# Kernel optimization log

Measured on AMD Instinct MI355X. Metric: run time of the kernel, lower is better.

Reference implementation:

```python
import jax, jax.numpy as jnp
import numpy as np

B, Q, S, D = 16, 2048, 2048, 128  # batch(*heads), q_len, kv seq_len, dim_q_k == dim_v


def setup_inputs() -> dict:
    key = jax.random.key(0)
    k1, k2, k3, k4 = jax.random.split(key, 4)
    value = jax.random.normal(k1, (B, S, D), dtype=jnp.float32)
    k_ = jax.random.normal(k2, (B, S, D), dtype=jnp.float32)
    query = jax.random.normal(k3, (B, Q, D), dtype=jnp.float32)
    mask = jax.random.bernoulli(k4, 0.5, (B, Q, S))  # True = illegal connection
    return {"value": value, "key": k_, "query": query, "mask": mask}


def reference(value, key, query, mask):
    scale = np.power(D, -0.5).astype(np.float32)
    # adjacency: [B, Q, S]
    adjacency = jnp.einsum('bqd,bsd->bqs', query, key) * scale
    adjacency = jnp.where(mask, -jnp.inf, adjacency)
    attention = jax.nn.softmax(adjacency, axis=2)
    out = jnp.einsum('bqs,bsd->bqd', attention, value)
    return (out, attention)
```

## Files before the change

### kernel.cpp

```cpp
#include <hip/hip_runtime.h>
#include <hip/hip_bf16.h>

#define B_ 16
#define Q_ 2048
#define S_ 2048
#define D_ 128
#define SCALE 0.08838834764831845f

typedef unsigned short ushort_t;
typedef unsigned long long u64_t;
typedef __attribute__((ext_vector_type(8))) __bf16 bf16x8;
typedef __attribute__((ext_vector_type(8))) short short8;
typedef __attribute__((ext_vector_type(4))) float floatx4;

static __device__ __forceinline__ ushort_t bf16_of_f32(float f) {
    __hip_bfloat16 h = __float2bfloat16(f);
    return *reinterpret_cast<ushort_t*>(&h);
}
static __device__ __forceinline__ float f32_of_bf16(ushort_t u) {
    return __uint_as_float(((unsigned int)u) << 16);
}

__global__ void detect_kernel(const unsigned int* __restrict__ m,
                              const unsigned int* __restrict__ q,
                              int* __restrict__ flags) {
    __shared__ int sI32, sF32, sF16, sCnt;
    int t = threadIdx.x;
    if (t == 0) { sI32 = 0; sF32 = 0; sF16 = 0; sCnt = 0; }
    __syncthreads();
    int notI32 = 0, notF32 = 0, notF16 = 0;
    for (int i = t; i < 1024; i += 256) {
        unsigned int v = m[i];
        if (v & ~1u) notI32 = 1;
        if (!(v == 0u || v == 0x3F800000u)) notF32 = 1;
        unsigned int h0 = v & 0xFFFFu, h1 = v >> 16;
        if (!(h0 == 0u || h0 == 0x3F80u || h0 == 0x3C00u)) notF16 = 1;
        if (!(h1 == 0u || h1 == 0x3F80u || h1 == 0x3C00u)) notF16 = 1;
    }
    int cnt = 0;
    for (int i = t; i < 4096; i += 256) {
        unsigned int lo = q[i] & 0xFFFFu;
        unsigned int e = (lo >> 7) & 0xFFu;
        if (lo == 0u || (e >= 100u && e <= 140u)) cnt++;
    }
    if (notI32) atomicOr(&sI32, 1);
    if (notF32) atomicOr(&sF32, 1);
    if (notF16) atomicOr(&sF16, 1);
    atomicAdd(&sCnt, cnt);
    __syncthreads();
    if (t == 0) {
        int w;
        if (!sI32)      w = 4;
        else if (!sF32) w = 4;
        else if (!sF16) w = 2;
        else            w = 1;
        flags[0] = w;
        flags[1] = (sCnt >= 3276) ? 0 : 1;
    }
}

__global__ void pack_mask_kernel(const void* __restrict__ maskp,
                                 const int* __restrict__ flags,
                                 u64_t* __restrict__ bits) {
    const int mw = flags[0];
    const size_t base = (size_t)blockIdx.x * (256 * 32);
    const int lane = threadIdx.x & 63;
    const int wid  = threadIdx.x >> 6;
    const unsigned int*  m32 = (const unsigned int*)maskp;
    const ushort_t*      m16 = (const ushort_t*)maskp;
    const unsigned char* m8  = (const unsigned char*)maskp;
    #pragma unroll 4
    for (int k = 0; k < 32; ++k) {
        int it = wid + 4 * k;
        size_t idx = base + (size_t)it * 64 + lane;
        bool mk;
        if (mw == 4)      mk = m32[idx] != 0u;
        else if (mw == 2) mk = m16[idx] != 0;
        else              mk = m8[idx]  != 0;
        u64_t b = __ballot(mk);
        if (lane == 0) bits[base / 64 + it] = b;
    }
}

__global__ void transpose_v_kernel(const void* __restrict__ Vraw,
                                   const int* __restrict__ flags,
                                   ushort_t* __restrict__ Vt) {
    __shared__ ushort_t t[32][33];
    const int dt = flags[1];
    int b = blockIdx.z;
    int sb = blockIdx.x * 32, db = blockIdx.y * 32;
    int x = threadIdx.x, y = threadIdx.y;
    ushort_t* Vtb = Vt + (size_t)b * D_ * S_;
    if (dt == 0) {
        const ushort_t* Vb = (const ushort_t*)Vraw + (size_t)b * S_ * D_;
        #pragma unroll
        for (int i = 0; i < 32; i += 8)
            t[y + i][x] = Vb[(size_t)(sb + y + i) * D_ + db + x];
    } else {
        const float* Vb = (const float*)Vraw + (size_t)b * S_ * D_;
        #pragma unroll
        for (int i = 0; i < 32; i += 8)
            t[y + i][x] = bf16_of_f32(Vb[(size_t)(sb + y + i) * D_ + db + x]);
    }
    __syncthreads();
    #pragma unroll
    for (int i = 0; i < 32; i += 8)
        Vtb[(size_t)(db + y + i) * S_ + sb + x] = t[x][y + i];
}

static __device__ __forceinline__ void stage_K(ushort_t (*Kl)[136],
                                               const void* Kraw, int dt,
                                               int b, int s0, int tid) {
    if (dt == 0) {
        const ushort_t* Kg = (const ushort_t*)Kraw;
        #pragma unroll
        for (int j = 0; j < 4; ++j) {
            int i = tid + 256 * j;
            int row = i >> 4, colg = i & 15;
            *(short8*)(&Kl[row][colg * 8]) =
                *(const short8*)(Kg + (size_t)(b * S_ + s0 + row) * D_ + colg * 8);
        }
    } else {
        const float* Kg = (const float*)Kraw;
        #pragma unroll
        for (int j = 0; j < 4; ++j) {
            int i = tid + 256 * j;
            int row = i >> 4, colg = i & 15;
            const float* src = Kg + (size_t)(b * S_ + s0 + row) * D_ + colg * 8;
            float4 f0 = *(const float4*)(src);
            float4 f1 = *(const float4*)(src + 4);
            short8 w;
            w[0] = (short)bf16_of_f32(f0.x); w[1] = (short)bf16_of_f32(f0.y);
            w[2] = (short)bf16_of_f32(f0.z); w[3] = (short)bf16_of_f32(f0.w);
            w[4] = (short)bf16_of_f32(f1.x); w[5] = (short)bf16_of_f32(f1.y);
            w[6] = (short)bf16_of_f32(f1.z); w[7] = (short)bf16_of_f32(f1.w);
            *(short8*)(&Kl[row][colg * 8]) = w;
        }
    }
}

__launch_bounds__(256, 2)
__global__ void attn_fused_kernel(const void* __restrict__ Kraw,
                                  const void* __restrict__ Qraw,
                                  const u64_t* __restrict__ bits,
                                  const int* __restrict__ flags,
                                  const ushort_t* __restrict__ Vt,
                                  void* __restrict__ out_base) {
    __shared__ ushort_t Kl[64][136];
    __shared__ ushort_t Vl[128][72];
    __shared__ ushort_t El[64][72];

    const int tid  = threadIdx.x;
    const int wave = tid >> 6;
    const int lane = tid & 63;
    const int quad = lane >> 4;
    const int c    = lane & 15;

    const int qt = blockIdx.x, b = blockIdx.y;
    const int q0 = qt * 64;
    const int dt = flags[1];

    ushort_t* outh  = (ushort_t*)out_base;
    float*    outf  = (float*)out_base;
    ushort_t* attnh = outh + (size_t)B_ * Q_ * D_;
    float*    attnf = outf + (size_t)B_ * Q_ * D_;

    const size_t rowbase = (size_t)b * Q_ + q0;
    const int myrow = wave * 16 + quad * 4;
    const u64_t* bitrow = bits + (((rowbase + myrow) * (size_t)S_) >> 6);

    bf16x8 qf[4];
    {
        const size_t qrow = rowbase + wave * 16 + c;
        if (dt == 0) {
            const ushort_t* p = (const ushort_t*)Qraw + qrow * D_;
            #pragma unroll
            for (int kk = 0; kk < 4; ++kk)
                qf[kk] = *(const bf16x8*)(p + kk * 32 + quad * 8);
        } else {
            const float* p = (const float*)Qraw + qrow * D_;
            #pragma unroll
            for (int kk = 0; kk < 4; ++kk) {
                float4 f0 = *(const float4*)(p + kk * 32 + quad * 8);
                float4 f1 = *(const float4*)(p + kk * 32 + quad * 8 + 4);
                bf16x8 w;
                w[0] = (__bf16)f0.x; w[1] = (__bf16)f0.y;
                w[2] = (__bf16)f0.z; w[3] = (__bf16)f0.w;
                w[4] = (__bf16)f1.x; w[5] = (__bf16)f1.y;
                w[6] = (__bf16)f1.z; w[7] = (__bf16)f1.w;
                qf[kk] = w;
            }
        }
    }

    floatx4 accO[8];
    #pragma unroll
    for (int i = 0; i < 8; ++i) accO[i] = (floatx4){0.f, 0.f, 0.f, 0.f};
    float lacc[4] = {0.f, 0.f, 0.f, 0.f};

    for (int s0 = 0; s0 < S_; s0 += 64) {
        u64_t bw[4];
        #pragma unroll
        for (int r = 0; r < 4; ++r) bw[r] = bitrow[r * 32 + (s0 >> 6)];

        __syncthreads();
        stage_K(Kl, Kraw, dt, b, s0, tid);
        #pragma unroll
        for (int j = 0; j < 4; ++j) {
            int i = tid + 256 * j;
            int row = i >> 3, colg = i & 7;
            *(short8*)(&Vl[row][colg * 8]) =
                *(const short8*)(Vt + (size_t)(b * D_ + row) * S_ + s0 + colg * 8);
        }
        __syncthreads();

        #pragma unroll
        for (int st = 0; st < 4; ++st) {
            floatx4 acc = (floatx4){0.f, 0.f, 0.f, 0.f};
            #pragma unroll
            for (int kk = 0; kk < 4; ++kk) {
                bf16x8 bf = *(const bf16x8*)(&Kl[st * 16 + c][kk * 32 + quad * 8]);
                acc = __builtin_amdgcn_mfma_f32_16x16x32_bf16(qf[kk], bf, acc, 0, 0, 0);
            }
            #pragma unroll
            for (int r = 0; r < 4; ++r) {
                bool masked = (bw[r] >> (st * 16 + c)) & 1ull;
                float e = masked ? 0.f : __expf(acc[r] * SCALE);
                lacc[r] += e;
                El[myrow + r][st * 16 + c] = bf16_of_f32(e);
            }
        }
        #pragma unroll
        for (int ks = 0; ks < 2; ++ks) {
            bf16x8 af = *(const bf16x8*)(&El[wave * 16 + c][ks * 32 + quad * 8]);
            #pragma unroll
            for (int nt = 0; nt < 8; ++nt) {
                bf16x8 bv = *(const bf16x8*)(&Vl[nt * 16 + c][ks * 32 + quad * 8]);
                accO[nt] = __builtin_amdgcn_mfma_f32_16x16x32_bf16(af, bv, accO[nt], 0, 0, 0);
            }
        }
    }

    float rcpl[4];
    #pragma unroll
    for (int r = 0; r < 4; ++r) {
        float v = lacc[r];
        v += __shfl_xor(v, 1); v += __shfl_xor(v, 2);
        v += __shfl_xor(v, 4); v += __shfl_xor(v, 8);
        rcpl[r] = 1.0f / fmaxf(v, 1e-30f);
    }

    #pragma unroll
    for (int r = 0; r < 4; ++r) {
        size_t orow = (rowbase + myrow + r) * D_;
        #pragma unroll
        for (int nt = 0; nt < 8; ++nt) {
            float v = accO[nt][r] * rcpl[r];
            if (dt == 0) outh[orow + nt * 16 + c] = bf16_of_f32(v);
            else         outf[orow + nt * 16 + c] = v;
        }
    }

    for (int s0 = 0; s0 < S_; s0 += 64) {
        u64_t bw[4];
        #pragma unroll
        for (int r = 0; r < 4; ++r) bw[r] = bitrow[r * 32 + (s0 >> 6)];

        __syncthreads();
        stage_K(Kl, Kraw, dt, b, s0, tid);
        __syncthreads();

        #pragma unroll
        for (int st = 0; st < 4; ++st) {
            floatx4 acc = (floatx4){0.f, 0.f, 0.f, 0.f};
            #pragma unroll
            for (int kk = 0; kk < 4; ++kk) {
                bf16x8 bf = *(const bf16x8*)(&Kl[st * 16 + c][kk * 32 + quad * 8]);
                acc = __builtin_amdgcn_mfma_f32_16x16x32_bf16(qf[kk], bf, acc, 0, 0, 0);
            }
            #pragma unroll
            for (int r = 0; r < 4; ++r) {
                bool masked = (bw[r] >> (st * 16 + c)) & 1ull;
                float e = masked ? 0.f : __expf(acc[r] * SCALE) * rcpl[r];
                El[myrow + r][st * 16 + c] = bf16_of_f32(e);
            }
        }
        __syncthreads();

        #pragma unroll
        for (int j = 0; j < 2; ++j) {
            int s = tid + 256 * j;
            int row = s >> 3, sc = s & 7;
            short8 v = *(short8*)(&El[row][sc * 8]);
            size_t gidx = (rowbase + row) * (size_t)S_ + s0 + sc * 8;
            if (dt == 0) {
                *(short8*)(attnh + gidx) = v;
            } else {
                float4 f0, f1;
                f0.x = f32_of_bf16((ushort_t)v[0]); f0.y = f32_of_bf16((ushort_t)v[1]);
                f0.z = f32_of_bf16((ushort_t)v[2]); f0.w = f32_of_bf16((ushort_t)v[3]);
                f1.x = f32_of_bf16((ushort_t)v[4]); f1.y = f32_of_bf16((ushort_t)v[5]);
                f1.z = f32_of_bf16((ushort_t)v[6]); f1.w = f32_of_bf16((ushort_t)v[7]);
                *(float4*)(attnf + gidx) = f0;
                *(float4*)(attnf + gidx + 4) = f1;
            }
        }
    }
}

extern "C" void kernel_launch(void* const* d_in, const int* in_sizes, int n_in,
                              void* d_out, int out_size, void* d_ws, size_t ws_size,
                              hipStream_t stream) {
    const void* Vraw = d_in[0];
    const void* Kraw = d_in[1];
    const void* Qraw = d_in[2];
    const void* maskp = d_in[3];

    char* ws = (char*)d_ws;
    int*  flags = (int*)ws;
    ushort_t* Vt = (ushort_t*)(ws + 256);
    u64_t* bits  = (u64_t*)(ws + 256 + (size_t)B_ * D_ * S_ * 2);

    detect_kernel<<<1, 256, 0, stream>>>((const unsigned int*)maskp,
                                         (const unsigned int*)Qraw, flags);
    pack_mask_kernel<<<(unsigned int)(((size_t)B_ * Q_ * S_) / 8192), 256, 0, stream>>>(
        maskp, flags, bits);
    transpose_v_kernel<<<dim3(S_ / 32, D_ / 32, B_), dim3(32, 8), 0, stream>>>(
        Vraw, flags, Vt);
    attn_fused_kernel<<<dim3(Q_ / 64, B_), 256, 0, stream>>>(
        Kraw, Qraw, bits, flags, Vt, d_out);
}
```

Measured before the change: 688.5 us.

## Fuse mask packing into attention kernel, pre-convert K to bf16, split S across wave pairs

Removes the separate mask-packing kernel. The fused kernel now stages raw mask tiles in shared memory during the first pass, uses them directly and writes packed bits for the second pass to reuse. K is converted to bf16 once by a new kernel, so both passes load bf16 K directly. Blocks grow to 512 threads, with wave pairs splitting each 64-column S tile and their partial row sums and outputs reduced through shared memory. This trades extra shared memory, more synchronisation and a cross-wave output reduction for fewer passes over the mask and K.

New measurement: 605.2 us. 12.1% less time.

```diff
diff --git a/kernel.cpp b/kernel.cpp
--- a/kernel.cpp
+++ b/kernel.cpp
@@ -59,27 +59,19 @@
     }
 }
 
-__global__ void pack_mask_kernel(const void* __restrict__ maskp,
-                                 const int* __restrict__ flags,
-                                 u64_t* __restrict__ bits) {
-    const int mw = flags[0];
-    const size_t base = (size_t)blockIdx.x * (256 * 32);
-    const int lane = threadIdx.x & 63;
-    const int wid  = threadIdx.x >> 6;
-    const unsigned int*  m32 = (const unsigned int*)maskp;
-    const ushort_t*      m16 = (const ushort_t*)maskp;
-    const unsigned char* m8  = (const unsigned char*)maskp;
-    #pragma unroll 4
-    for (int k = 0; k < 32; ++k) {
-        int it = wid + 4 * k;
-        size_t idx = base + (size_t)it * 64 + lane;
-        bool mk;
-        if (mw == 4)      mk = m32[idx] != 0u;
-        else if (mw == 2) mk = m16[idx] != 0;
-        else              mk = m8[idx]  != 0;
-        u64_t b = __ballot(mk);
-        if (lane == 0) bits[base / 64 + it] = b;
-    }
+__global__ void convert_bf16_kernel(const float* __restrict__ src,
+                                    const int* __restrict__ flags,
+                                    ushort_t* __restrict__ dst) {
+    if (flags[1] == 0) return;
+    size_t i = ((size_t)blockIdx.x * 256 + threadIdx.x) * 8;
+    float4 f0 = *(const float4*)(src + i);
+    float4 f1 = *(const float4*)(src + i + 4);
+    short8 w;
+    w[0] = (short)bf16_of_f32(f0.x); w[1] = (short)bf16_of_f32(f0.y);
+    w[2] = (short)bf16_of_f32(f0.z); w[3] = (short)bf16_of_f32(f0.w);
+    w[4] = (short)bf16_of_f32(f1.x); w[5] = (short)bf16_of_f32(f1.y);
+    w[6] = (short)bf16_of_f32(f1.z); w[7] = (short)bf16_of_f32(f1.w);
+    *(short8*)(dst + i) = w;
 }
 
 __global__ void transpose_v_kernel(const void* __restrict__ Vraw,
@@ -108,57 +100,37 @@
         Vtb[(size_t)(db + y + i) * S_ + sb + x] = t[x][y + i];
 }
 
-static __device__ __forceinline__ void stage_K(ushort_t (*Kl)[136],
-                                               const void* Kraw, int dt,
-                                               int b, int s0, int tid) {
-    if (dt == 0) {
-        const ushort_t* Kg = (const ushort_t*)Kraw;
-        #pragma unroll
-        for (int j = 0; j < 4; ++j) {
-            int i = tid + 256 * j;
-            int row = i >> 4, colg = i & 15;
-            *(short8*)(&Kl[row][colg * 8]) =
-                *(const short8*)(Kg + (size_t)(b * S_ + s0 + row) * D_ + colg * 8);
-        }
-    } else {
-        const float* Kg = (const float*)Kraw;
-        #pragma unroll
-        for (int j = 0; j < 4; ++j) {
-            int i = tid + 256 * j;
-            int row = i >> 4, colg = i & 15;
-            const float* src = Kg + (size_t)(b * S_ + s0 + row) * D_ + colg * 8;
-            float4 f0 = *(const float4*)(src);
-            float4 f1 = *(const float4*)(src + 4);
-            short8 w;
-            w[0] = (short)bf16_of_f32(f0.x); w[1] = (short)bf16_of_f32(f0.y);
-            w[2] = (short)bf16_of_f32(f0.z); w[3] = (short)bf16_of_f32(f0.w);
-            w[4] = (short)bf16_of_f32(f1.x); w[5] = (short)bf16_of_f32(f1.y);
-            w[6] = (short)bf16_of_f32(f1.z); w[7] = (short)bf16_of_f32(f1.w);
-            *(short8*)(&Kl[row][colg * 8]) = w;
-        }
-    }
-}
-
-__launch_bounds__(256, 2)
+__launch_bounds__(512, 4)
 __global__ void attn_fused_kernel(const void* __restrict__ Kraw,
+                                  const ushort_t* __restrict__ Kbf,
                                   const void* __restrict__ Qraw,
-                                  const u64_t* __restrict__ bits,
+                                  const void* __restrict__ maskp,
                                   const int* __restrict__ flags,
                                   const ushort_t* __restrict__ Vt,
+                                  u64_t* __restrict__ bits,
                                   void* __restrict__ out_base) {
-    __shared__ ushort_t Kl[64][136];
-    __shared__ ushort_t Vl[128][72];
-    __shared__ ushort_t El[64][72];
+    __shared__ __align__(16) char smem[62976];
+    ushort_t (*Kl)[136] = (ushort_t(*)[136])smem;
+    ushort_t (*Vl)[72]  = (ushort_t(*)[72])(smem + 17408);
+    float    (*Ob)[132] = (float(*)[132])smem;
+    ushort_t (*El)[72]  = (ushort_t(*)[72])(smem + 35840);
+    char*    Mlb        = smem + 45056;
+    float*   lpart      = (float*)(smem + 62464);
 
     const int tid  = threadIdx.x;
     const int wave = tid >> 6;
     const int lane = tid & 63;
     const int quad = lane >> 4;
     const int c    = lane & 15;
+    const int sh   = wave & 1;
+    const int wg   = wave >> 1;
 
     const int qt = blockIdx.x, b = blockIdx.y;
     const int q0 = qt * 64;
+    const int mw = flags[0];
     const int dt = flags[1];
+
+    const ushort_t* Kp = dt ? Kbf : (const ushort_t*)Kraw;
 
     ushort_t* outh  = (ushort_t*)out_base;
     float*    outf  = (float*)out_base;
@@ -166,12 +138,11 @@
     float*    attnf = outf + (size_t)B_ * Q_ * D_;
 
     const size_t rowbase = (size_t)b * Q_ + q0;
-    const int myrow = wave * 16 + quad * 4;
-    const u64_t* bitrow = bits + (((rowbase + myrow) * (size_t)S_) >> 6);
+    const int myrow = wg * 16 + quad * 4;
 
     bf16x8 qf[4];
     {
-        const size_t qrow = rowbase + wave * 16 + c;
+        const size_t qrow = rowbase + wg * 16 + c;
         if (dt == 0) {
             const ushort_t* p = (const ushort_t*)Qraw + qrow * D_;
             #pragma unroll
@@ -199,23 +170,59 @@
     float lacc[4] = {0.f, 0.f, 0.f, 0.f};
 
     for (int s0 = 0; s0 < S_; s0 += 64) {
-        u64_t bw[4];
-        #pragma unroll
-        for (int r = 0; r < 4; ++r) bw[r] = bitrow[r * 32 + (s0 >> 6)];
-
-        __syncthreads();
-        stage_K(Kl, Kraw, dt, b, s0, tid);
-        #pragma unroll
-        for (int j = 0; j < 4; ++j) {
-            int i = tid + 256 * j;
-            int row = i >> 3, colg = i & 7;
-            *(short8*)(&Vl[row][colg * 8]) =
-                *(const short8*)(Vt + (size_t)(b * D_ + row) * S_ + s0 + colg * 8);
-        }
-        __syncthreads();
-
-        #pragma unroll
-        for (int st = 0; st < 4; ++st) {
+        __syncthreads();
+        #pragma unroll
+        for (int j = 0; j < 2; ++j) {
+            int i = tid + 512 * j;
+            int row = i >> 4, cg = i & 15;
+            *(short8*)(&Kl[row][cg * 8]) =
+                *(const short8*)(Kp + (size_t)(b * S_ + s0 + row) * D_ + cg * 8);
+        }
+        #pragma unroll
+        for (int j = 0; j < 2; ++j) {
+            int i = tid + 512 * j;
+            int row = i >> 3, cg = i & 7;
+            *(short8*)(&Vl[row][cg * 8]) =
+                *(const short8*)(Vt + (size_t)(b * D_ + row) * S_ + s0 + cg * 8);
+        }
+        if (mw == 4) {
+            const unsigned int* Mg = (const unsigned int*)maskp;
+            #pragma unroll
+            for (int j = 0; j < 2; ++j) {
+                int i = tid + 512 * j;
+                int row = i >> 4, c4 = i & 15;
+                *(uint4*)(Mlb + row * 272 + c4 * 16) =
+                    *(const uint4*)(Mg + (rowbase + row) * (size_t)S_ + s0 + c4 * 4);
+            }
+        } else if (mw == 2) {
+            const ushort_t* Mg = (const ushort_t*)maskp;
+            int row = tid >> 3, c16 = tid & 7;
+            *(uint4*)(Mlb + row * 272 + c16 * 16) =
+                *(const uint4*)(Mg + (rowbase + row) * (size_t)S_ + s0 + c16 * 8);
+        } else {
+            if (tid < 256) {
+                const unsigned char* Mg = (const unsigned char*)maskp;
+                int row = tid >> 2, c16 = tid & 3;
+                *(uint4*)(Mlb + row * 272 + c16 * 16) =
+                    *(const uint4*)(Mg + (rowbase + row) * (size_t)S_ + s0 + c16 * 16);
+            }
+        }
+        __syncthreads();
+
+        #pragma unroll
+        for (int k = 0; k < 8; ++k) {
+            int row = wave * 8 + k;
+            bool mk;
+            if (mw == 4)      mk = ((const unsigned int*)(Mlb + row * 272))[lane] != 0u;
+            else if (mw == 2) mk = ((const ushort_t*)(Mlb + row * 272))[lane] != 0;
+            else              mk = ((const unsigned char*)(Mlb + row * 272))[lane] != 0;
+            u64_t bm = __ballot(mk);
+            if (lane == 0) bits[(rowbase + row) * 32 + (s0 >> 6)] = bm;
+        }
+
+        #pragma unroll
+        for (int sti = 0; sti < 2; ++sti) {
+            const int st = sh * 2 + sti;
             floatx4 acc = (floatx4){0.f, 0.f, 0.f, 0.f};
             #pragma unroll
             for (int kk = 0; kk < 4; ++kk) {
@@ -224,54 +231,105 @@
             }
             #pragma unroll
             for (int r = 0; r < 4; ++r) {
-                bool masked = (bw[r] >> (st * 16 + c)) & 1ull;
+                const int row = myrow + r, col = st * 16 + c;
+                bool masked;
+                if (mw == 4)      masked = ((const unsigned int*)(Mlb + row * 272))[col] != 0u;
+                else if (mw == 2) masked = ((const ushort_t*)(Mlb + row * 272))[col] != 0;
+                else              masked = ((const unsigned char*)(Mlb + row * 272))[col] != 0;
                 float e = masked ? 0.f : __expf(acc[r] * SCALE);
                 lacc[r] += e;
-                El[myrow + r][st * 16 + c] = bf16_of_f32(e);
-            }
-        }
-        #pragma unroll
-        for (int ks = 0; ks < 2; ++ks) {
-            bf16x8 af = *(const bf16x8*)(&El[wave * 16 + c][ks * 32 + quad * 8]);
+                El[row][col] = bf16_of_f32(e);
+            }
+        }
+        {
+            bf16x8 af = *(const bf16x8*)(&El[wg * 16 + c][sh * 32 + quad * 8]);
             #pragma unroll
             for (int nt = 0; nt < 8; ++nt) {
-                bf16x8 bv = *(const bf16x8*)(&Vl[nt * 16 + c][ks * 32 + quad * 8]);
+                bf16x8 bv = *(const bf16x8*)(&Vl[nt * 16 + c][sh * 32 + quad * 8]);
                 accO[nt] = __builtin_amdgcn_mfma_f32_16x16x32_bf16(af, bv, accO[nt], 0, 0, 0);
             }
         }
     }
 
-    float rcpl[4];
     #pragma unroll
     for (int r = 0; r < 4; ++r) {
         float v = lacc[r];
         v += __shfl_xor(v, 1); v += __shfl_xor(v, 2);
         v += __shfl_xor(v, 4); v += __shfl_xor(v, 8);
-        rcpl[r] = 1.0f / fmaxf(v, 1e-30f);
-    }
-
+        lacc[r] = v;
+    }
+    __syncthreads();
+    if (c == 0) {
+        #pragma unroll
+        for (int r = 0; r < 4; ++r) lpart[sh * 64 + myrow + r] = lacc[r];
+    }
+    __syncthreads();
+    float rcpl[4];
     #pragma unroll
-    for (int r = 0; r < 4; ++r) {
-        size_t orow = (rowbase + myrow + r) * D_;
-        #pragma unroll
-        for (int nt = 0; nt < 8; ++nt) {
-            float v = accO[nt][r] * rcpl[r];
-            if (dt == 0) outh[orow + nt * 16 + c] = bf16_of_f32(v);
-            else         outf[orow + nt * 16 + c] = v;
+    for (int r = 0; r < 4; ++r)
+        rcpl[r] = 1.0f / fmaxf(lpart[myrow + r] + lpart[64 + myrow + r], 1e-30f);
+
+    if (sh == 0) {
+        #pragma unroll
+        for (int r = 0; r < 4; ++r)
+            #pragma unroll
+            for (int nt = 0; nt < 8; ++nt)
+                Ob[myrow + r][nt * 16 + c] = accO[nt][r];
+    }
+    __syncthreads();
+    if (sh == 1) {
+        #pragma unroll
+        for (int r = 0; r < 4; ++r)
+            #pragma unroll
+            for (int nt = 0; nt < 8; ++nt)
+                Ob[myrow + r][nt * 16 + c] += accO[nt][r];
+    }
+    __syncthreads();
+    {
+        const int row = tid >> 3, dc = tid & 7;
+        float rcp = 1.0f / fmaxf(lpart[row] + lpart[64 + row], 1e-30f);
+        size_t obase = (rowbase + row) * (size_t)D_ + dc * 16;
+        if (dt == 0) {
+            short8 w0, w1;
+            #pragma unroll
+            for (int k = 0; k < 8; ++k) {
+                w0[k] = (short)bf16_of_f32(Ob[row][dc * 16 + k] * rcp);
+                w1[k] = (short)bf16_of_f32(Ob[row][dc * 16 + 8 + k] * rcp);
+            }
+            *(short8*)(outh + obase) = w0;
+            *(short8*)(outh + obase + 8) = w1;
+        } else {
+            #pragma unroll
+            for (int g = 0; g < 4; ++g) {
+                float4 f;
+                f.x = Ob[row][dc * 16 + g * 4 + 0] * rcp;
+                f.y = Ob[row][dc * 16 + g * 4 + 1] * rcp;
+                f.z = Ob[row][dc * 16 + g * 4 + 2] * rcp;
+                f.w = Ob[row][dc * 16 + g * 4 + 3] * rcp;
+                *(float4*)(outf + obase + g * 4) = f;
+            }
         }
     }
 
     for (int s0 = 0; s0 < S_; s0 += 64) {
+        __syncthreads();
+        #pragma unroll
+        for (int j = 0; j < 2; ++j) {
+            int i = tid + 512 * j;
+            int row = i >> 4, cg = i & 15;
+            *(short8*)(&Kl[row][cg * 8]) =
+                *(const short8*)(Kp + (size_t)(b * S_ + s0 + row) * D_ + cg * 8);
+        }
+        __syncthreads();
+
         u64_t bw[4];
         #pragma unroll
-        for (int r = 0; r < 4; ++r) bw[r] = bitrow[r * 32 + (s0 >> 6)];
-
-        __syncthreads();
-        stage_K(Kl, Kraw, dt, b, s0, tid);
-        __syncthreads();
-
-        #pragma unroll
-        for (int st = 0; st < 4; ++st) {
+        for (int r = 0; r < 4; ++r)
+            bw[r] = bits[(rowbase + myrow + r) * 32 + (s0 >> 6)];
+
+        #pragma unroll
+        for (int sti = 0; sti < 2; ++sti) {
+            const int st = sh * 2 + sti;
             floatx4 acc = (floatx4){0.f, 0.f, 0.f, 0.f};
             #pragma unroll
             for (int kk = 0; kk < 4; ++kk) {
@@ -287,10 +345,8 @@
         }
         __syncthreads();
 
-        #pragma unroll
-        for (int j = 0; j < 2; ++j) {
-            int s = tid + 256 * j;
-            int row = s >> 3, sc = s & 7;
+        {
+            const int row = tid >> 3, sc = tid & 7;
             short8 v = *(short8*)(&El[row][sc * 8]);
             size_t gidx = (rowbase + row) * (size_t)S_ + s0 + sc * 8;
             if (dt == 0) {
@@ -317,16 +373,17 @@
     const void* maskp = d_in[3];
 
     char* ws = (char*)d_ws;
-    int*  flags = (int*)ws;
-    ushort_t* Vt = (ushort_t*)(ws + 256);
-    u64_t* bits  = (u64_t*)(ws + 256 + (size_t)B_ * D_ * S_ * 2);
+    int*  flags   = (int*)ws;
+    ushort_t* Vt  = (ushort_t*)(ws + 256);
+    u64_t* bits   = (u64_t*)(ws + 256 + 8388608);
+    ushort_t* Kbf = (ushort_t*)(ws + 256 + 2 * 8388608);
 
     detect_kernel<<<1, 256, 0, stream>>>((const unsigned int*)maskp,
                                          (const unsigned int*)Qraw, flags);
-    pack_mask_kernel<<<(unsigned int)(((size_t)B_ * Q_ * S_) / 8192), 256, 0, stream>>>(
-        maskp, flags, bits);
+    convert_bf16_kernel<<<(B_ * S_ * D_) / 2048, 256, 0, stream>>>(
+        (const float*)Kraw, flags, Kbf);
     transpose_v_kernel<<<dim3(S_ / 32, D_ / 32, B_), dim3(32, 8), 0, stream>>>(
         Vraw, flags, Vt);
-    attn_fused_kernel<<<dim3(Q_ / 64, B_), 256, 0, stream>>>(
-        Kraw, Qraw, bits, flags, Vt, d_out);
-}
+    attn_fused_kernel<<<dim3(Q_ / 64, B_), 512, 0, stream>>>(
+        Kraw, Kbf, Qraw, maskp, flags, Vt, bits, d_out);
+}
```
